# Performance work log

Measured on AMD Instinct MI355X. Metric: run time of the kernel, lower is better.

## Reference

```python
import jax, jax.numpy as jnp
import numpy as np

D = 768; H = 12; DH = 64; P = 16; G = 14; NP = 196; L = 197
LD = 4; GD = 12          # local / latent depths
RL = 12; RG = 8          # tokens merged per layer (total_merge // depth)
B = 8
EPS = 1e-6


def layernorm(x, g, b):
    mu = x.mean(-1, keepdims=True)
    v = ((x - mu) ** 2).mean(-1, keepdims=True)
    return (x - mu) / jnp.sqrt(v + EPS) * g + b


def attention(x, size, qkv_w, qkv_b, pw, pb):
    # proportional attention: logits += log(token size)
    Bn, N, _ = x.shape
    qkv = (x @ qkv_w + qkv_b).reshape(Bn, N, 3, H, DH)
    q, k, v = (qkv[:, :, i].transpose(0, 2, 1, 3) for i in range(3))  # bhnd
    logits = jnp.einsum('bhqd,bhkd->bhqk', q, k) * (DH ** -0.5)
    logits = logits + jnp.log(size)[:, None, None, :, 0]
    a = jax.nn.softmax(logits, axis=-1)
    o = jnp.einsum('bhqk,bhkd->bhqd', a, v).transpose(0, 2, 1, 3).reshape(Bn, N, D)
    return o @ pw + pb, k.mean(1)  # metric = mean key over heads


def tome_merge(x, size, metric, r, tok_map):
    # ToMe bipartite soft matching + weighted-average merge + source-map update
    Bn, N, _ = x.shape
    t1, t2 = (N + 1) // 2, N // 2
    m = metric / jnp.linalg.norm(metric, axis=-1, keepdims=True)
    scores = jnp.einsum('bid,bjd->bij', m[:, ::2], m[:, 1::2])
    scores = scores.at[:, 0, :].set(-jnp.inf)  # protect cls token
    node_max, node_idx = scores.max(-1), scores.argmax(-1).astype(jnp.int32)
    order = jnp.argsort(-node_max, axis=-1).astype(jnp.int32)
    src_idx = order[:, :r]
    unm_idx = jnp.sort(order[:, r:], axis=-1)  # cls stays first
    dst_idx = jnp.take_along_axis(node_idx, src_idx, axis=1)
    bi = jnp.arange(Bn)[:, None]

    def merge_sum(v):
        a, b = v[:, ::2], v[:, 1::2]
        unm = jnp.take_along_axis(a, unm_idx[..., None], axis=1)
        s = jnp.take_along_axis(a, src_idx[..., None], axis=1)
        b = b.at[bi, dst_idx].add(s)
        return jnp.concatenate([unm, b], axis=1)

    new_size = merge_sum(size)
    new_x = merge_sum(x * size) / new_size
    # per-step old->new index map, then compose with running source map
    pos_a = jnp.zeros((Bn, t1), jnp.int32)
    pos_a = pos_a.at[bi, unm_idx].set(jnp.arange(t1 - r, dtype=jnp.int32))
    pos_a = pos_a.at[bi, src_idx].set((t1 - r) + dst_idx)
    step = jnp.zeros((Bn, N), jnp.int32)
    step = step.at[:, ::2].set(pos_a)
    step = step.at[:, 1::2].set((t1 - r) + jnp.arange(t2, dtype=jnp.int32)[None])
    return new_x, new_size, jnp.take_along_axis(step, tok_map, axis=1)


def encode(x, size, tok_map, r, p):
    ln1g, ln1b, qw, qb, pw, pb, ln2g, ln2b, f1w, f1b, f2w, f2b = p
    for i in range(ln1g.shape[0]):
        a, metric = attention(layernorm(x, ln1g[i], ln1b[i]), size, qw[i], qb[i], pw[i], pb[i])
        x = x + a
        if r > 0:
            x, size, tok_map = tome_merge(x, size, metric, r, tok_map)
        h = layernorm(x, ln2g[i], ln2b[i])
        x = x + (jax.nn.gelu(h @ f1w[i] + f1b[i], approximate=False) @ f2w[i] + f2b[i])
    return x, size, tok_map


def setup_inputs() -> dict:
    key = jax.random.key(0)
    ks = iter(jax.random.split(key, 64))
    def w(shape):
        return jax.random.normal(next(ks), shape, jnp.float32) * 0.02
    def blocks(d, pre):
        return {pre + 'ln1g': jnp.ones((d, D)), pre + 'ln1b': jnp.zeros((d, D)),
                pre + 'qkv_w': w((d, D, 3 * D)), pre + 'qkv_b': jnp.zeros((d, 3 * D)),
                pre + 'proj_w': w((d, D, D)), pre + 'proj_b': jnp.zeros((d, D)),
                pre + 'ln2g': jnp.ones((d, D)), pre + 'ln2b': jnp.zeros((d, D)),
                pre + 'fc1w': w((d, D, 4 * D)), pre + 'fc1b': jnp.zeros((d, 4 * D)),
                pre + 'fc2w': w((d, 4 * D, D)), pre + 'fc2b': jnp.zeros((d, D))}
    inp = dict(x=jax.random.normal(next(ks), (B, 3, 224, 224), jnp.float32),
               patch_w=w((3 * P * P, D)), patch_b=jnp.zeros((D,)),
               cls_tok=w((1, 1, D)), pos_emb=w((1, L, D)),
               l_ng=jnp.ones((D,)), l_nb=jnp.zeros((D,)),
               g_ng=jnp.ones((D,)), g_nb=jnp.zeros((D,)),
               head_w=w((D, 10)), head_b=jnp.zeros((10,)))
    inp.update(blocks(LD, 'l_'))
    inp.update(blocks(GD, 'g_'))
    return inp


def reference(x, patch_w, patch_b, cls_tok, pos_emb,
              l_ln1g, l_ln1b, l_qkv_w, l_qkv_b, l_proj_w, l_proj_b,
              l_ln2g, l_ln2b, l_fc1w, l_fc1b, l_fc2w, l_fc2b, l_ng, l_nb,
              g_ln1g, g_ln1b, g_qkv_w, g_qkv_b, g_proj_w, g_proj_b,
              g_ln2g, g_ln2b, g_fc1w, g_fc1b, g_fc2w, g_fc2b, g_ng, g_nb,
              head_w, head_b):
    Bn = x.shape[0]
    # non-overlapping 16x16 patchify == conv stride 16
    patches = x.reshape(Bn, 3, G, P, G, P).transpose(0, 2, 4, 1, 3, 5).reshape(Bn, NP, 3 * P * P)
    t = patches @ patch_w + patch_b
    t = jnp.concatenate([jnp.broadcast_to(cls_tok, (Bn, 1, D)), t], axis=1) + pos_emb
    size = jnp.ones((Bn, L, 1), t.dtype)
    tmap = jnp.broadcast_to(jnp.arange(L, dtype=jnp.int32)[None], (Bn, L))  # token_map_for_dtem
    lp = (l_ln1g, l_ln1b, l_qkv_w, l_qkv_b, l_proj_w, l_proj_b, l_ln2g, l_ln2b, l_fc1w, l_fc1b, l_fc2w, l_fc2b)
    xl, size, tmap = encode(t, size, tmap, RL, lp)   # local encoder: 197 -> 149 tokens
    xl = layernorm(xl, l_ng, l_nb)
    N1 = xl.shape[1]
    smap = jnp.broadcast_to(jnp.arange(N1, dtype=jnp.int32)[None], (Bn, N1))  # latent source_map
    gp = (g_ln1g, g_ln1b, g_qkv_w, g_qkv_b, g_proj_w, g_proj_b, g_ln2g, g_ln2b, g_fc1w, g_fc1b, g_fc2w, g_fc2b)
    xg, size, smap = encode(xl, size, smap, RG, gp)  # latent encoder: 149 -> 53 tokens
    xg = layernorm(xg, g_ng, g_nb)
    xr = jnp.take_along_axis(xg, smap[..., None], axis=1)   # token_unmerge_from_map (ToMe)
    xf = jnp.take_along_axis(xr, tmap[..., None], axis=1)   # token_unmerge_from_map_for_dtem
    return xf[:, 0] @ head_w + head_b  # cls token -> logits (B, 10)
```

## Files before the change

kernel.cpp:

```cpp
#include <hip/hip_runtime.h>
#include <math.h>

#define NB 8
#define SD 768
#define NHEAD 12
#define LMAX 197
#define QBLK 32
#define KBLK 64

typedef __attribute__((ext_vector_type(8))) short bf16x8;
typedef __attribute__((ext_vector_type(4))) float f32x4;
typedef const __attribute__((address_space(1))) unsigned int gu32_t;
typedef __attribute__((address_space(3))) unsigned int lu32_t;

static __device__ __forceinline__ float geluf(float x){
    return 0.5f*x*(1.0f+erff(x*0.70710678118654752440f));
}

static __device__ __forceinline__ void split_bf16(float v, ushort& h, ushort& l){
    uint u = __float_as_uint(v);
    uint hb = (u + 0x7FFFu + ((u>>16)&1u)) >> 16;
    h = (ushort)hb;
    float rem = v - __uint_as_float(hb<<16);
    uint u2 = __float_as_uint(rem);
    l = (ushort)((u2 + 0x7FFFu + ((u2>>16)&1u)) >> 16);
}

__global__ __launch_bounds__(256) void wconv(const float* __restrict__ W,
        ushort* __restrict__ Hi, ushort* __restrict__ Lo, int K, int Nc)
{
    __shared__ float tile[32][33];
    int z = blockIdx.z;
    const float* Wz = W + (size_t)z*K*Nc;
    ushort* Hz = Hi + (size_t)z*Nc*K;
    ushort* Lz = Lo + (size_t)z*Nc*K;
    int n0 = blockIdx.x*32, k0 = blockIdx.y*32;
    int tx = threadIdx.x&31, ty = threadIdx.x>>5;
    #pragma unroll
    for (int i=0;i<32;i+=8) tile[ty+i][tx] = Wz[(size_t)(k0+ty+i)*Nc + n0+tx];
    __syncthreads();
    #pragma unroll
    for (int i=0;i<32;i+=8){
        float v = tile[tx][ty+i];
        ushort h,l; split_bf16(v,h,l);
        size_t o = (size_t)(n0+ty+i)*K + k0+tx;
        Hz[o]=h; Lz[o]=l;
    }
}

template<int EPI, int SPLITK>
__global__ __launch_bounds__(256) void gemm_mfma(const ushort* __restrict__ AHi,
        const ushort* __restrict__ ALo, const ushort* __restrict__ WHi,
        const ushort* __restrict__ WLo, const float* __restrict__ bias,
        const float* __restrict__ R, float* __restrict__ C,
        ushort* __restrict__ CHi, ushort* __restrict__ CLo,
        float* __restrict__ Part, int M, int Nc, int K, int ntok, int gx)
{
    __shared__ ushort sAhi[4096], sAlo[4096], sBhi[4096], sBlo[4096];
    const int t = threadIdx.x;
    const int nwg = gridDim.x;
    const int qc = nwg>>3, rc = nwg&7;
    const int xcd = blockIdx.x & 7, jj = blockIdx.x >> 3;
    const int wid = (xcd<rc ? xcd*(qc+1) : rc*(qc+1)+(xcd-rc)*qc) + jj;
    const int bx = wid % gx;
    const int t2 = wid / gx;
    const int gy = nwg/(gx*SPLITK);
    const int by = t2 % gy;
    const int bz = t2 / gy;

    const int w = t>>6, l = t&63, lr = l&15, lg = l>>4;
    const int wr = w>>1, wc = w&1;
    const int srow = t>>3;
    const uint kchunk = (uint)(((l&7) ^ (l>>3)) << 4);

    const int Ks = K/SPLITK;
    const int kbeg = bz*Ks;
    const int nt = Ks/64;

    const char* pA[2][2]; const char* pW[2][2];
    #pragma unroll
    for (int p=0;p<2;p++){
        int row = p*32 + srow;
        int ar = by*64 + row; if (ar >= M) ar = M-1;
        int b = ar/ntok; int n = ar - b*ntok;
        size_t ab = ((size_t)(b*LMAX+n)*K + kbeg)*2 + kchunk;
        size_t wb = ((size_t)(bx*64+row)*K + kbeg)*2 + kchunk;
        pA[p][0] = (const char*)AHi + ab;  pA[p][1] = (const char*)ALo + ab;
        pW[p][0] = (const char*)WHi + wb;  pW[p][1] = (const char*)WLo + wb;
    }

    f32x4 acc[2][2];
    #pragma unroll
    for (int i=0;i<2;i++)
        #pragma unroll
        for (int j=0;j<2;j++) acc[i][j] = (f32x4){0.f,0.f,0.f,0.f};

    auto stage = [&](int kt){
        size_t ko = (size_t)kt*128;
        #pragma unroll
        for (int p=0;p<2;p++){
            uint lb = (uint)((p*32 + w*8)*64);
            __builtin_amdgcn_global_load_lds((gu32_t*)(pA[p][0]+ko), (lu32_t*)&sAhi[lb], 16, 0, 0);
            __builtin_amdgcn_global_load_lds((gu32_t*)(pA[p][1]+ko), (lu32_t*)&sAlo[lb], 16, 0, 0);
            __builtin_amdgcn_global_load_lds((gu32_t*)(pW[p][0]+ko), (lu32_t*)&sBhi[lb], 16, 0, 0);
            __builtin_amdgcn_global_load_lds((gu32_t*)(pW[p][1]+ko), (lu32_t*)&sBlo[lb], 16, 0, 0);
        }
    };

    stage(0);
    for (int kt=0; kt<nt; ++kt){
        asm volatile("s_waitcnt vmcnt(0)" ::: "memory");
        __builtin_amdgcn_s_barrier();
        #pragma unroll
        for (int kk=0;kk<2;kk++){
            bf16x8 ah[2], al[2], bh[2], bl[2];
            #pragma unroll
            for (int m=0;m<2;m++){
                int row = wr*32 + m*16 + lr;
                uint off = (uint)((row*128 + kk*64 + lg*16) ^ ((row&7)<<4));
                ah[m] = *(const bf16x8*)((const char*)sAhi + off);
                al[m] = *(const bf16x8*)((const char*)sAlo + off);
            }
            #pragma unroll
            for (int n=0;n<2;n++){
                int col = wc*32 + n*16 + lr;
                uint off = (uint)((col*128 + kk*64 + lg*16) ^ ((col&7)<<4));
                bh[n] = *(const bf16x8*)((const char*)sBhi + off);
                bl[n] = *(const bf16x8*)((const char*)sBlo + off);
            }
            #pragma unroll
            for (int m=0;m<2;m++)
                #pragma unroll
                for (int n=0;n<2;n++){
                    acc[m][n] = __builtin_amdgcn_mfma_f32_16x16x32_bf16(ah[m], bh[n], acc[m][n], 0,0,0);
                    acc[m][n] = __builtin_amdgcn_mfma_f32_16x16x32_bf16(ah[m], bl[n], acc[m][n], 0,0,0);
                    acc[m][n] = __builtin_amdgcn_mfma_f32_16x16x32_bf16(al[m], bh[n], acc[m][n], 0,0,0);
                }
        }
        __builtin_amdgcn_s_barrier();
        if (kt+1 < nt) stage(kt+1);
    }

    if (SPLITK > 1){
        float* Pz = Part + (size_t)bz*M*Nc;
        #pragma unroll
        for (int m=0;m<2;m++){
            #pragma unroll
            for (int n=0;n<2;n++){
                int gcol = bx*64 + wc*32 + n*16 + lr;
                #pragma unroll
                for (int r=0;r<4;r++){
                    int grow = by*64 + wr*32 + m*16 + lg*4 + r;
                    if (grow >= M) continue;
                    Pz[(size_t)grow*Nc + gcol] = acc[m][n][r];
                }
            }
        }
    } else {
        #pragma unroll
        for (int m=0;m<2;m++){
            #pragma unroll
            for (int n=0;n<2;n++){
                int gcol = bx*64 + wc*32 + n*16 + lr;
                float bv = bias[gcol];
                #pragma unroll
                for (int r=0;r<4;r++){
                    int grow = by*64 + wr*32 + m*16 + lg*4 + r;
                    if (grow >= M) continue;
                    int b = grow/ntok; int ni = grow - b*ntok;
                    size_t off = (size_t)(b*LMAX+ni)*Nc + gcol;
                    float v = acc[m][n][r] + bv;
                    if (EPI==1){
                        v = geluf(v);
                        ushort h,lo; split_bf16(v,h,lo);
                        CHi[off]=h; CLo[off]=lo;
                    } else {
                        if (EPI==2) v += R[off];
                        C[off] = v;
                    }
                }
            }
        }
    }
}

__global__ __launch_bounds__(256) void reduce_k(const float* __restrict__ P,
        const float* __restrict__ bias, const float* __restrict__ R,
        float* __restrict__ C, int M, int Nc, int S, int ntok)
{
    int idx = blockIdx.x*256 + threadIdx.x;
    int tot = M*(Nc/4);
    if (idx >= tot) return;
    int grow = idx/(Nc/4), c4 = idx - grow*(Nc/4);
    size_t po = (size_t)grow*Nc + c4*4;
    float4 a = *(const float4*)(P + po);
    for (int s=1;s<S;s++){
        float4 v = *(const float4*)(P + (size_t)s*M*Nc + po);
        a.x+=v.x; a.y+=v.y; a.z+=v.z; a.w+=v.w;
    }
    int b = grow/ntok, n = grow - b*ntok;
    size_t off = (size_t)(b*LMAX+n)*Nc + c4*4;
    float4 bv = *(const float4*)(bias + c4*4);
    float4 rv = *(const float4*)(R + off);
    float4 o;
    o.x=a.x+bv.x+rv.x; o.y=a.y+bv.y+rv.y; o.z=a.z+bv.z+rv.z; o.w=a.w+bv.w+rv.w;
    *(float4*)(C + off) = o;
}

__device__ __forceinline__ float block_sum256(float v){
    __shared__ float red[4];
    for (int o=32;o>0;o>>=1) v += __shfl_down(v,o,64);
    int t=threadIdx.x;
    if ((t&63)==0) red[t>>6]=v;
    __syncthreads();
    float r = red[0]+red[1]+red[2]+red[3];
    __syncthreads();
    return r;
}

__global__ __launch_bounds__(256) void ln_split(const float* __restrict__ X,
        const float* __restrict__ gam, const float* __restrict__ bet,
        ushort* __restrict__ YHi, ushort* __restrict__ YLo)
{
    int n = blockIdx.x, b = blockIdx.y, t = threadIdx.x;
    const float* xr = X + ((size_t)(b*LMAX+n))*SD;
    size_t ro = ((size_t)(b*LMAX+n))*SD;
    float v0=xr[t], v1=xr[t+256], v2=xr[t+512];
    float mu = block_sum256(v0+v1+v2) * (1.0f/768.0f);
    float d0=v0-mu, d1=v1-mu, d2=v2-mu;
    float var = block_sum256(d0*d0+d1*d1+d2*d2) * (1.0f/768.0f);
    float rs = rsqrtf(var + 1e-6f);
    float y0 = d0*rs*gam[t]     + bet[t];
    float y1 = d1*rs*gam[t+256] + bet[t+256];
    float y2 = d2*rs*gam[t+512] + bet[t+512];
    ushort h,lo;
    split_bf16(y0,h,lo); YHi[ro+t]=h;     YLo[ro+t]=lo;
    split_bf16(y1,h,lo); YHi[ro+t+256]=h; YLo[ro+t+256]=lo;
    split_bf16(y2,h,lo); YHi[ro+t+512]=h; YLo[ro+t+512]=lo;
}

__global__ __launch_bounds__(256) void ln_kernel(const float* __restrict__ X,
        const float* __restrict__ gam, const float* __restrict__ bet,
        float* __restrict__ Y)
{
    int n = blockIdx.x, b = blockIdx.y, t = threadIdx.x;
    const float* xr = X + ((size_t)(b*LMAX+n))*SD;
    float* yr = Y + ((size_t)(b*LMAX+n))*SD;
    float v0=xr[t], v1=xr[t+256], v2=xr[t+512];
    float mu = block_sum256(v0+v1+v2) * (1.0f/768.0f);
    float d0=v0-mu, d1=v1-mu, d2=v2-mu;
    float var = block_sum256(d0*d0+d1*d1+d2*d2) * (1.0f/768.0f);
    float rs = rsqrtf(var + 1e-6f);
    yr[t]     = d0*rs*gam[t]     + bet[t];
    yr[t+256] = d1*rs*gam[t+256] + bet[t+256];
    yr[t+512] = d2*rs*gam[t+512] + bet[t+512];
}

__global__ __launch_bounds__(256) void attn_tile(const float* __restrict__ QKV,
        const float* __restrict__ SZ, ushort* __restrict__ OHi,
        ushort* __restrict__ OLo, int N)
{
    const int q0 = blockIdx.x*QBLK;
    const int h = blockIdx.y, b = blockIdx.z, t = threadIdx.x;
    __shared__ float Qs[QBLK][68];
    __shared__ float KVs[KBLK][68];
    __shared__ float Ls[QBLK][200];
    __shared__ float szl[KBLK];
    __shared__ float invs[QBLK];

    {
        int row = t>>3, seg = t&7;
        int q = q0 + row;
        if (q < N){
            const float* src = QKV + ((size_t)(b*LMAX+q))*2304 + h*64 + seg*8;
            *(float4*)&Qs[row][seg*8]   = *(const float4*)src;
            *(float4*)&Qs[row][seg*8+4] = *(const float4*)(src+4);
        } else {
            float4 z = make_float4(0.f,0.f,0.f,0.f);
            *(float4*)&Qs[row][seg*8]   = z;
            *(float4*)&Qs[row][seg*8+4] = z;
        }
    }
    const int tq = t>>3, tk = t&7;
    const int nkt = (N+KBLK-1)/KBLK;

    for (int kt=0; kt<nkt; ++kt){
        int kbase = kt*KBLK;
        __syncthreads();
        {
            int row = t>>2, seg = t&3;
            int ktok = kbase + row;
            float4 a,b4,c,d4;
            if (ktok < N){
                const float* src = QKV + ((size_t)(b*LMAX+ktok))*2304 + 768 + h*64 + seg*16;
                a=*(const float4*)src; b4=*(const float4*)(src+4);
                c=*(const float4*)(src+8); d4=*(const float4*)(src+12);
            } else {
                a=b4=c=d4=make_float4(0.f,0.f,0.f,0.f);
            }
            *(float4*)&KVs[row][seg*16]   =a;
            *(float4*)&KVs[row][seg*16+4] =b4;
            *(float4*)&KVs[row][seg*16+8] =c;
            *(float4*)&KVs[row][seg*16+12]=d4;
            if (t < KBLK){
                int kk2 = kbase + t;
                szl[t] = (kk2<N) ? logf(SZ[b*LMAX+kk2]) : 0.f;
            }
        }
        __syncthreads();
        float acc[8];
        #pragma unroll
        for (int j=0;j<8;j++) acc[j]=0.f;
        #pragma unroll 4
        for (int d4=0; d4<16; ++d4){
            float4 qv = *(const float4*)&Qs[tq][d4*4];
            #pragma unroll
            for (int j=0;j<8;j++){
                float4 kv = *(const float4*)&KVs[tk+8*j][d4*4];
                acc[j] += qv.x*kv.x + qv.y*kv.y + qv.z*kv.z + qv.w*kv.w;
            }
        }
        #pragma unroll
        for (int j=0;j<8;j++){
            int kk = kbase + tk + 8*j;
            if (kk < N) Ls[tq][kk] = acc[j]*0.125f + szl[tk+8*j];
        }
    }
    __syncthreads();

    {
        float m = -INFINITY;
        for (int k=tk;k<N;k+=8) m = fmaxf(m, Ls[tq][k]);
        #pragma unroll
        for (int o=1;o<8;o<<=1) m = fmaxf(m, __shfl_xor(m,o,64));
        float s = 0.f;
        for (int k=tk;k<N;k+=8){
            float p = expf(Ls[tq][k]-m);
            Ls[tq][k]=p; s+=p;
        }
        #pragma unroll
        for (int o=1;o<8;o<<=1) s += __shfl_xor(s,o,64);
        if (tk==0) invs[tq] = 1.0f/s;
    }

    float o0[8];
    #pragma unroll
    for (int i=0;i<8;i++) o0[i]=0.f;
    for (int kt=0; kt<nkt; ++kt){
        int kbase = kt*KBLK;
        __syncthreads();
        {
            int row = t>>2, seg = t&3;
            int ktok = kbase + row;
            float4 a,b4,c,d4;
            if (ktok < N){
                const float* src = QKV + ((size_t)(b*LMAX+ktok))*2304 + 1536 + h*64 + seg*16;
                a=*(const float4*)src; b4=*(const float4*)(src+4);
                c=*(const float4*)(src+8); d4=*(const float4*)(src+12);
            } else {
                a=b4=c=d4=make_float4(0.f,0.f,0.f,0.f);
            }
            *(float4*)&KVs[row][seg*16]   =a;
            *(float4*)&KVs[row][seg*16+4] =b4;
            *(float4*)&KVs[row][seg*16+8] =c;
            *(float4*)&KVs[row][seg*16+12]=d4;
        }
        __syncthreads();
        int kmax = N - kbase; if (kmax > KBLK) kmax = KBLK;
        for (int kk=0; kk<kmax; ++kk){
            float p = Ls[tq][kbase+kk];
            float4 v0 = *(const float4*)&KVs[kk][tk*8];
            float4 v1 = *(const float4*)&KVs[kk][tk*8+4];
            o0[0]+=p*v0.x; o0[1]+=p*v0.y; o0[2]+=p*v0.z; o0[3]+=p*v0.w;
            o0[4]+=p*v1.x; o0[5]+=p*v1.y; o0[6]+=p*v1.z; o0[7]+=p*v1.w;
        }
    }
    int q = q0 + tq;
    if (q < N){
        float inv = invs[tq];
        ushort hh[8], ll[8];
        #pragma unroll
        for (int i=0;i<8;i++){ split_bf16(o0[i]*inv, hh[i], ll[i]); }
        size_t o = ((size_t)(b*LMAX+q))*SD + h*64 + tk*8;
        *(ushort4*)(OHi+o)   = make_ushort4(hh[0],hh[1],hh[2],hh[3]);
        *(ushort4*)(OHi+o+4) = make_ushort4(hh[4],hh[5],hh[6],hh[7]);
        *(ushort4*)(OLo+o)   = make_ushort4(ll[0],ll[1],ll[2],ll[3]);
        *(ushort4*)(OLo+o+4) = make_ushort4(ll[4],ll[5],ll[6],ll[7]);
    }
}

__global__ void metric_k(const float* __restrict__ QKV, float* __restrict__ MET)
{
    const int n = blockIdx.x, b = blockIdx.y, d = threadIdx.x;
    const float* base = QKV + ((size_t)(b*LMAX+n))*2304 + 768 + d;
    float s=0.f;
    #pragma unroll
    for (int h=0;h<12;h++) s += base[h*64];
    s *= (1.0f/12.0f);
    float sq = s*s;
    for (int o=32;o>0;o>>=1) sq += __shfl_down(sq,o,64);
    float nrm = sqrtf(__shfl(sq,0,64));
    MET[((size_t)(b*LMAX+n))*64 + d] = s/nrm;
}

__global__ __launch_bounds__(128) void scores_k(const float* __restrict__ MET,
        float* __restrict__ NMAX, int* __restrict__ NIDX, int t2)
{
    const int i = blockIdx.x, b = blockIdx.y, t = threadIdx.x;
    __shared__ float ma[64];
    __shared__ float vals[128];
    __shared__ int idxs[128];
    if (t<64) ma[t] = MET[((size_t)(b*LMAX+2*i))*64+t];
    __syncthreads();
    float val = -INFINITY;
    if (t<t2 && i>0){
        const float* mb = MET + ((size_t)(b*LMAX+2*t+1))*64;
        float dot=0.f;
        #pragma unroll 8
        for (int dd=0;dd<64;dd++) dot += ma[dd]*mb[dd];
        val = dot;
    }
    vals[t]=val; idxs[t]=t; __syncthreads();
    for (int s=64;s>0;s>>=1){
        if (t<s){
            float v2=vals[t+s], v1=vals[t]; int i2=idxs[t+s];
            if (v2>v1 || (v2==v1 && i2<idxs[t])){ vals[t]=v2; idxs[t]=i2; }
        }
        __syncthreads();
    }
    if (t==0){ NMAX[b*128+i]=vals[0]; NIDX[b*128+i]=idxs[0]; }
}

__global__ __launch_bounds__(128) void plan_k(const float* __restrict__ NMAX,
        const int* __restrict__ NIDX, int* __restrict__ SRC, int* __restrict__ DST,
        int* __restrict__ STEP, int* __restrict__ INV, int t1, int t2, int r)
{
    const int b = blockIdx.x, i = threadIdx.x;
    __shared__ float nm[128];
    __shared__ int issrc[128];
    nm[i] = (i<t1) ? NMAX[b*128+i] : INFINITY;
    __syncthreads();
    int rank=0, is=0, ni=0;
    if (i<t1){
        float m = nm[i];
        for (int j=0;j<t1;j++){ float a=nm[j]; if (a>m || (a==m && j<i)) rank++; }
        is = (rank<r) ? 1:0;
        ni = NIDX[b*128+i];
    }
    issrc[i]=is; __syncthreads();
    if (i<t1){
        if (is){ SRC[b*16+rank]=i; DST[b*16+rank]=ni; STEP[b*LMAX+2*i] = t1-r+ni; }
        else {
            int cnt=0;
            for (int j=0;j<i;j++) cnt += 1-issrc[j];
            STEP[b*LMAX+2*i]=cnt;
            INV[b*LMAX+cnt]=2*i;
        }
    }
    if (i<t2){ STEP[b*LMAX+2*i+1]=t1-r+i; INV[b*LMAX+(t1-r)+i]=2*i+1; }
}

__global__ __launch_bounds__(256) void merge_fused(const float* __restrict__ X,
        const float* __restrict__ SZ, const int* __restrict__ INV,
        const int* __restrict__ SRC, const int* __restrict__ DST,
        float* __restrict__ XO, float* __restrict__ SZO, int t1, int r)
{
    int p = blockIdx.x, b = blockIdx.y, t = threadIdx.x;
    int base = t1 - r;
    float acc0, acc1, acc2, snew;
    if (p < base){
        int tok = INV[b*LMAX+p];
        float s = SZ[b*LMAX+tok];
        const float* xr = X + (size_t)(b*LMAX+tok)*SD;
        acc0=xr[t]*s; acc1=xr[t+256]*s; acc2=xr[t+512]*s; snew=s;
    } else {
        int d = p - base;
        int tok = 2*d+1;
        float s = SZ[b*LMAX+tok];
        const float* xr = X + (size_t)(b*LMAX+tok)*SD;
        acc0=xr[t]*s; acc1=xr[t+256]*s; acc2=xr[t+512]*s; snew=s;
        for (int k=0;k<r;k++){
            if (DST[b*16+k]==d){
                int st = 2*SRC[b*16+k];
                float ss = SZ[b*LMAX+st];
                const float* xs = X + (size_t)(b*LMAX+st)*SD;
                acc0+=xs[t]*ss; acc1+=xs[t+256]*ss; acc2+=xs[t+512]*ss; snew+=ss;
            }
        }
    }
    float inv = 1.0f/snew;
    float* o = XO + (size_t)(b*LMAX+p)*SD;
    o[t]=acc0*inv; o[t+256]=acc1*inv; o[t+512]=acc2*inv;
    if (t==0) SZO[b*LMAX+p]=snew;
}

__global__ void map_upd(int* __restrict__ MAP, const int* __restrict__ STEP, int mlen)
{
    int i = blockIdx.x*256+threadIdx.x;
    if (i >= NB*mlen) return;
    int b=i/mlen, t=i-b*mlen;
    MAP[b*LMAX+t] = STEP[b*LMAX + MAP[b*LMAX+t]];
}

__global__ void patchify(const float* __restrict__ X, ushort* __restrict__ PHi,
        ushort* __restrict__ PLo)
{
    size_t i = (size_t)blockIdx.x*256 + threadIdx.x;
    if (i >= (size_t)NB*196*768) return;
    int f = i % 768; size_t q = i/768; int p = q % 196; int b = q/196;
    int c = f >> 8, py = (f>>4)&15, px = f&15;
    int gy = p/14, gx = p - gy*14;
    float v = X[(((size_t)b*3 + c)*224 + gy*16+py)*224 + gx*16+px];
    ushort h,l; split_bf16(v,h,l);
    size_t o = ((size_t)(b*LMAX+p))*768 + f;
    PHi[o]=h; PLo[o]=l;
}

__global__ void assemble(const float* __restrict__ T, const float* __restrict__ cls,
        const float* __restrict__ pos, float* __restrict__ Xo)
{
    size_t i = (size_t)blockIdx.x*256 + threadIdx.x;
    if (i >= (size_t)NB*LMAX*768) return;
    int d = i % 768; size_t q = i/768; int n = q % LMAX; int b = q/LMAX;
    float v = (n==0) ? cls[d] : T[((size_t)(b*LMAX+n-1))*768+d];
    Xo[((size_t)(b*LMAX+n))*768+d] = v + pos[n*768+d];
}

__global__ void init_state(float* __restrict__ SZ, int* __restrict__ TMAP, int* __restrict__ SMAP)
{
    int i = blockIdx.x*256+threadIdx.x;
    if (i >= NB*LMAX) return;
    SZ[i]=1.0f;
    int n=i%LMAX;
    TMAP[i]=n;
    if (n<149) SMAP[i]=n;
}

__global__ void head_k(const float* __restrict__ XG, const int* __restrict__ SMAP,
        const int* __restrict__ TMAP, const float* __restrict__ HW,
        const float* __restrict__ HB, float* __restrict__ OUT)
{
    int t = threadIdx.x;
    if (t>=80) return;
    int b=t/10, o=t-b*10;
    int row = SMAP[b*LMAX + TMAP[b*LMAX]];
    const float* xr = XG + ((size_t)(b*LMAX+row))*SD;
    float acc = HB[o];
    for (int d=0;d<SD;d++) acc += xr[d]*HW[d*10+o];
    OUT[b*10+o]=acc;
}

extern "C" void kernel_launch(void* const* d_in, const int* in_sizes, int n_in,
                              void* d_out, int out_size, void* d_ws, size_t ws_size,
                              hipStream_t stream)
{
    const float* x_in    = (const float*)d_in[0];
    const float* patch_w = (const float*)d_in[1];
    const float* patch_b = (const float*)d_in[2];
    const float* cls     = (const float*)d_in[3];
    const float* pos     = (const float*)d_in[4];
    const float* l_ng    = (const float*)d_in[5];
    const float* l_nb    = (const float*)d_in[6];
    const float* g_ng    = (const float*)d_in[7];
    const float* g_nb    = (const float*)d_in[8];
    const float* head_w  = (const float*)d_in[9];
    const float* head_b  = (const float*)d_in[10];
    const float* L[12];  for (int i=0;i<12;i++) L[i]  = (const float*)d_in[11+i];
    const float* Gp[12]; for (int i=0;i<12;i++) Gp[i] = (const float*)d_in[23+i];
    float* out = (float*)d_out;

    float* fp = (float*)d_ws;
    float* xA      = fp; fp += (size_t)NB*LMAX*SD;
    float* xB      = fp; fp += (size_t)NB*LMAX*SD;
    float* qkvbuf  = fp; fp += (size_t)NB*LMAX*2304;
    float* metricbuf=fp; fp += (size_t)NB*LMAX*64;
    float* partbuf = fp; fp += (size_t)4*NB*LMAX*SD;
    float* szA     = fp; fp += NB*LMAX;
    float* szB     = fp; fp += NB*LMAX;
    float* nodemax = fp; fp += NB*128;
    int* ip = (int*)fp;
    int* tmap    = ip; ip += NB*LMAX;
    int* smap    = ip; ip += NB*LMAX;
    int* stepbuf = ip; ip += NB*LMAX;
    int* invrow  = ip; ip += NB*LMAX;
    int* nodeidx = ip; ip += NB*128;
    int* srcs    = ip; ip += NB*16;
    int* dsts    = ip; ip += NB*16;
    uintptr_t up = ((uintptr_t)ip + 15) & ~(uintptr_t)15;
    ushort* sp = (ushort*)up;
    ushort* lnHi = sp; sp += (size_t)NB*LMAX*SD;
    ushort* lnLo = sp; sp += (size_t)NB*LMAX*SD;
    ushort* oHi  = sp; sp += (size_t)NB*LMAX*SD;
    ushort* oLo  = sp; sp += (size_t)NB*LMAX*SD;
    ushort* hHi  = sp; sp += (size_t)NB*LMAX*3072;
    ushort* hLo  = sp; sp += (size_t)NB*LMAX*3072;
    ushort* pHi  = sp; sp += (size_t)NB*LMAX*SD;
    ushort* pLo  = sp; sp += (size_t)NB*LMAX*SD;
    ushort* patchHi = sp; sp += (size_t)768*768;
    ushort* patchLo = sp; sp += (size_t)768*768;
    ushort* qkvHi = sp; sp += (size_t)4*768*2304;
    ushort* qkvLo = sp; sp += (size_t)4*768*2304;
    ushort* projHi= sp; sp += (size_t)4*768*768;
    ushort* projLo= sp; sp += (size_t)4*768*768;
    ushort* fc1Hi = sp; sp += (size_t)4*768*3072;
    ushort* fc1Lo = sp; sp += (size_t)4*768*3072;
    ushort* fc2Hi = sp; sp += (size_t)4*3072*768;
    ushort* fc2Lo = sp; sp += (size_t)4*3072*768;

    float *xc = xA, *xn = xB, *szc = szA, *szn = szB;

    auto conv_chunk = [&](const float* qw, const float* pw, const float* f1w,
                          const float* f2w, int nz)
    {
        wconv<<<dim3(2304/32,768/32,nz),256,0,stream>>>(qw, qkvHi, qkvLo, SD, 2304);
        wconv<<<dim3(768/32,768/32,nz),256,0,stream>>>(pw, projHi, projLo, SD, SD);
        wconv<<<dim3(3072/32,768/32,nz),256,0,stream>>>(f1w, fc1Hi, fc1Lo, SD, 3072);
        wconv<<<dim3(768/32,3072/32,nz),256,0,stream>>>(f2w, fc2Hi, fc2Lo, 3072, SD);
    };

    auto run_block = [&](const float* ln1g, const float* ln1b, const float* qb,
                         const float* pb, const float* ln2g, const float* ln2b,
                         const float* f1b, const float* f2b,
                         int slot, int N, int r, int* mp, int mlen)
    {
        int M = NB*N;
        int Mt = (M+63)/64;
        const ushort* qH = qkvHi + (size_t)slot*768*2304;
        const ushort* qL = qkvLo + (size_t)slot*768*2304;
        const ushort* pH = projHi + (size_t)slot*768*768;
        const ushort* pL = projLo + (size_t)slot*768*768;
        const ushort* f1H = fc1Hi + (size_t)slot*768*3072;
        const ushort* f1L = fc1Lo + (size_t)slot*768*3072;
        const ushort* f2H = fc2Hi + (size_t)slot*3072*768;
        const ushort* f2L = fc2Lo + (size_t)slot*3072*768;

        ln_split<<<dim3(N,NB),256,0,stream>>>(xc, ln1g, ln1b, lnHi, lnLo);
        gemm_mfma<0,1><<<36*Mt,256,0,stream>>>(lnHi, lnLo, qH, qL, qb, nullptr, qkvbuf, nullptr, nullptr, nullptr, M, 2304, SD, N, 36);
        attn_tile<<<dim3((N+QBLK-1)/QBLK,NHEAD,NB),256,0,stream>>>(qkvbuf, szc, oHi, oLo, N);
        metric_k<<<dim3(N,NB),64,0,stream>>>(qkvbuf, metricbuf);
        gemm_mfma<0,4><<<12*Mt*4,256,0,stream>>>(oHi, oLo, pH, pL, nullptr, nullptr, nullptr, nullptr, nullptr, partbuf, M, SD, SD, N, 12);
        reduce_k<<<(M*(SD/4)+255)/256,256,0,stream>>>(partbuf, pb, xc, xc, M, SD, 4, N);
        int t1=(N+1)/2, t2=N/2, Nn=N-r;
        scores_k<<<dim3(t1,NB),128,0,stream>>>(metricbuf, nodemax, nodeidx, t2);
        plan_k<<<NB,128,0,stream>>>(nodemax, nodeidx, srcs, dsts, stepbuf, invrow, t1, t2, r);
        merge_fused<<<dim3(Nn,NB),256,0,stream>>>(xc, szc, invrow, srcs, dsts, xn, szn, t1, r);
        map_upd<<<(NB*mlen+255)/256,256,0,stream>>>(mp, stepbuf, mlen);
        int M2 = NB*Nn;
        int M2t = (M2+63)/64;
        ln_split<<<dim3(Nn,NB),256,0,stream>>>(xn, ln2g, ln2b, lnHi, lnLo);
        gemm_mfma<1,1><<<48*M2t,256,0,stream>>>(lnHi, lnLo, f1H, f1L, f1b, nullptr, nullptr, hHi, hLo, nullptr, M2, 3072, SD, Nn, 48);
        gemm_mfma<0,4><<<12*M2t*4,256,0,stream>>>(hHi, hLo, f2H, f2L, nullptr, nullptr, nullptr, nullptr, nullptr, partbuf, M2, SD, 3072, Nn, 12);
        reduce_k<<<(M2*(SD/4)+255)/256,256,0,stream>>>(partbuf, f2b, xn, xn, M2, SD, 4, Nn);
        float* tf; tf=xc; xc=xn; xn=tf; tf=szc; szc=szn; szn=tf;
    };

    {
        int tot = NB*196*768;
        patchify<<<(tot+255)/256,256,0,stream>>>(x_in, pHi, pLo);
        wconv<<<dim3(768/32,768/32,1),256,0,stream>>>(patch_w, patchHi, patchLo, SD, SD);
        gemm_mfma<0,1><<<12*((NB*196+63)/64),256,0,stream>>>(pHi, pLo, patchHi, patchLo, patch_b, nullptr, qkvbuf, nullptr, nullptr, nullptr, NB*196, SD, SD, 196, 12);
        int tot2 = NB*LMAX*768;
        assemble<<<(tot2+255)/256,256,0,stream>>>(qkvbuf, cls, pos, xc);
        init_state<<<(NB*LMAX+255)/256,256,0,stream>>>(szc, tmap, smap);
    }

    conv_chunk(L[2], L[4], L[8], L[10], 4);
    int N = 197;
    for (int i=0;i<4;i++){
        run_block(L[0]+i*768, L[1]+i*768, L[3]+(size_t)i*2304,
                  L[5]+(size_t)i*768, L[6]+i*768, L[7]+i*768,
                  L[9]+(size_t)i*3072, L[11]+(size_t)i*768,
                  i, N, 12, tmap, 197);
        N -= 12;
    }
    ln_kernel<<<dim3(N,NB),256,0,stream>>>(xc, l_ng, l_nb, xc);

    for (int c=0;c<3;c++){
        conv_chunk(Gp[2]+(size_t)(4*c)*768*2304, Gp[4]+(size_t)(4*c)*768*768,
                   Gp[8]+(size_t)(4*c)*768*3072, Gp[10]+(size_t)(4*c)*3072*768, 4);
        for (int j=0;j<4;j++){
            int i = 4*c+j;
            run_block(Gp[0]+i*768, Gp[1]+i*768, Gp[3]+(size_t)i*2304,
                      Gp[5]+(size_t)i*768, Gp[6]+i*768, Gp[7]+i*768,
                      Gp[9]+(size_t)i*3072, Gp[11]+(size_t)i*768,
                      j, N, 8, smap, 149);
            N -= 8;
        }
    }
    ln_kernel<<<dim3(N,NB),256,0,stream>>>(xc, g_ng, g_nb, qkvbuf);
    head_k<<<1,128,0,stream>>>(qkvbuf, smap, tmap, head_w, head_b, out);
}
```

Measured before the change: 2.857 ms.

## Double-buffer GEMM LDS tiles with K=32 stages and prefetch next tile

The split bf16 GEMM now keeps two LDS buffers of 32-wide K tiles. It issues the global-to-LDS loads for the next tile before computing on the current one, waiting only on the older loads. The aim is to hide global memory latency that the previous single-buffer load-then-compute loop exposed. In exchange there are twice as many barrier-separated iterations. The XOR swizzle on LDS addresses is removed, which may introduce bank conflicts on the fragment reads.

```diff
diff --git a/kernel.cpp b/kernel.cpp
--- a/kernel.cpp
+++ b/kernel.cpp
@@ -56,7 +56,8 @@
         ushort* __restrict__ CHi, ushort* __restrict__ CLo,
         float* __restrict__ Part, int M, int Nc, int K, int ntok, int gx)
 {
-    __shared__ ushort sAhi[4096], sAlo[4096], sBhi[4096], sBlo[4096];
+    __shared__ __align__(16) ushort sAhi[2][2048], sAlo[2][2048];
+    __shared__ __align__(16) ushort sBhi[2][2048], sBlo[2][2048];
     const int t = threadIdx.x;
     const int nwg = gridDim.x;
     const int qc = nwg>>3, rc = nwg&7;
@@ -70,24 +71,21 @@
 
     const int w = t>>6, l = t&63, lr = l&15, lg = l>>4;
     const int wr = w>>1, wc = w&1;
-    const int srow = t>>3;
-    const uint kchunk = (uint)(((l&7) ^ (l>>3)) << 4);
 
     const int Ks = K/SPLITK;
     const int kbeg = bz*Ks;
-    const int nt = Ks/64;
-
-    const char* pA[2][2]; const char* pW[2][2];
-    #pragma unroll
-    for (int p=0;p<2;p++){
-        int row = p*32 + srow;
-        int ar = by*64 + row; if (ar >= M) ar = M-1;
-        int b = ar/ntok; int n = ar - b*ntok;
-        size_t ab = ((size_t)(b*LMAX+n)*K + kbeg)*2 + kchunk;
-        size_t wb = ((size_t)(bx*64+row)*K + kbeg)*2 + kchunk;
-        pA[p][0] = (const char*)AHi + ab;  pA[p][1] = (const char*)ALo + ab;
-        pW[p][0] = (const char*)WHi + wb;  pW[p][1] = (const char*)WLo + wb;
-    }
+    const int nt = Ks/32;
+
+    const int srow = t>>2;
+    const uint schunk = (uint)((t&3)*16);
+    int ar = by*64 + srow; if (ar >= M) ar = M-1;
+    int ab_ = ar/ntok; int an_ = ar - ab_*ntok;
+    size_t aoff = ((size_t)(ab_*LMAX+an_)*K + kbeg)*2 + schunk;
+    size_t woff = ((size_t)(bx*64+srow)*K + kbeg)*2 + schunk;
+    const char* pAh = (const char*)AHi + aoff;
+    const char* pAl = (const char*)ALo + aoff;
+    const char* pWh = (const char*)WHi + woff;
+    const char* pWl = (const char*)WLo + woff;
 
     f32x4 acc[2][2];
     #pragma unroll
@@ -95,50 +93,49 @@
         #pragma unroll
         for (int j=0;j<2;j++) acc[i][j] = (f32x4){0.f,0.f,0.f,0.f};
 
-    auto stage = [&](int kt){
-        size_t ko = (size_t)kt*128;
-        #pragma unroll
-        for (int p=0;p<2;p++){
-            uint lb = (uint)((p*32 + w*8)*64);
-            __builtin_amdgcn_global_load_lds((gu32_t*)(pA[p][0]+ko), (lu32_t*)&sAhi[lb], 16, 0, 0);
-            __builtin_amdgcn_global_load_lds((gu32_t*)(pA[p][1]+ko), (lu32_t*)&sAlo[lb], 16, 0, 0);
-            __builtin_amdgcn_global_load_lds((gu32_t*)(pW[p][0]+ko), (lu32_t*)&sBhi[lb], 16, 0, 0);
-            __builtin_amdgcn_global_load_lds((gu32_t*)(pW[p][1]+ko), (lu32_t*)&sBlo[lb], 16, 0, 0);
-        }
+    const uint wb = (uint)(w*512);
+
+    auto stage = [&](int bf, int kt){
+        size_t ko = (size_t)kt*64;
+        __builtin_amdgcn_global_load_lds((gu32_t*)(pAh+ko), (lu32_t*)&sAhi[bf][wb], 16, 0, 0);
+        __builtin_amdgcn_global_load_lds((gu32_t*)(pAl+ko), (lu32_t*)&sAlo[bf][wb], 16, 0, 0);
+        __builtin_amdgcn_global_load_lds((gu32_t*)(pWh+ko), (lu32_t*)&sBhi[bf][wb], 16, 0, 0);
+        __builtin_amdgcn_global_load_lds((gu32_t*)(pWl+ko), (lu32_t*)&sBlo[bf][wb], 16, 0, 0);
     };
 
-    stage(0);
+    int buf = 0;
+    stage(0, 0);
     for (int kt=0; kt<nt; ++kt){
-        asm volatile("s_waitcnt vmcnt(0)" ::: "memory");
+        if (kt+1 < nt){
+            stage(buf^1, kt+1);
+            asm volatile("s_waitcnt vmcnt(4)" ::: "memory");
+        } else {
+            asm volatile("s_waitcnt vmcnt(0)" ::: "memory");
+        }
         __builtin_amdgcn_s_barrier();
-        #pragma unroll
-        for (int kk=0;kk<2;kk++){
-            bf16x8 ah[2], al[2], bh[2], bl[2];
-            #pragma unroll
-            for (int m=0;m<2;m++){
-                int row = wr*32 + m*16 + lr;
-                uint off = (uint)((row*128 + kk*64 + lg*16) ^ ((row&7)<<4));
-                ah[m] = *(const bf16x8*)((const char*)sAhi + off);
-                al[m] = *(const bf16x8*)((const char*)sAlo + off);
-            }
+        bf16x8 ah[2], al[2], bh[2], bl[2];
+        #pragma unroll
+        for (int m=0;m<2;m++){
+            uint off = (uint)((wr*32 + m*16 + lr)*64 + lg*16);
+            ah[m] = *(const bf16x8*)((const char*)&sAhi[buf][0] + off);
+            al[m] = *(const bf16x8*)((const char*)&sAlo[buf][0] + off);
+        }
+        #pragma unroll
+        for (int n=0;n<2;n++){
+            uint off = (uint)((wc*32 + n*16 + lr)*64 + lg*16);
+            bh[n] = *(const bf16x8*)((const char*)&sBhi[buf][0] + off);
+            bl[n] = *(const bf16x8*)((const char*)&sBlo[buf][0] + off);
+        }
+        #pragma unroll
+        for (int m=0;m<2;m++)
             #pragma unroll
             for (int n=0;n<2;n++){
-                int col = wc*32 + n*16 + lr;
-                uint off = (uint)((col*128 + kk*64 + lg*16) ^ ((col&7)<<4));
-                bh[n] = *(const bf16x8*)((const char*)sBhi + off);
-                bl[n] = *(const bf16x8*)((const char*)sBlo + off);
-            }
-            #pragma unroll
-            for (int m=0;m<2;m++)
-                #pragma unroll
-                for (int n=0;n<2;n++){
-                    acc[m][n] = __builtin_amdgcn_mfma_f32_16x16x32_bf16(ah[m], bh[n], acc[m][n], 0,0,0);
-                    acc[m][n] = __builtin_amdgcn_mfma_f32_16x16x32_bf16(ah[m], bl[n], acc[m][n], 0,0,0);
-                    acc[m][n] = __builtin_amdgcn_mfma_f32_16x16x32_bf16(al[m], bh[n], acc[m][n], 0,0,0);
-                }
-        }
+                acc[m][n] = __builtin_amdgcn_mfma_f32_16x16x32_bf16(ah[m], bh[n], acc[m][n], 0,0,0);
+                acc[m][n] = __builtin_amdgcn_mfma_f32_16x16x32_bf16(ah[m], bl[n], acc[m][n], 0,0,0);
+                acc[m][n] = __builtin_amdgcn_mfma_f32_16x16x32_bf16(al[m], bh[n], acc[m][n], 0,0,0);
+            }
         __builtin_amdgcn_s_barrier();
-        if (kt+1 < nt) stage(kt+1);
+        buf ^= 1;
     }
 
     if (SPLITK > 1){
```

Result: faster. 2.753 ms (-3.7%).
